# Kernel optimization log

Measured on AMD Instinct MI355X. Metric: run time of the kernel, lower is better.

Reference implementation:

```python
import jax, jax.numpy as jnp
import numpy as np

D_MODEL = 256
N_LEVELS = 4
N_HEADS = 8
N_POINTS = 4
D_HEAD = D_MODEL // N_HEADS  # 32
BATCH = 8
SHAPES = np.array([[64, 64], [32, 32], [16, 16], [8, 8]], dtype=np.int32)
LEN_IN = int((SHAPES[:, 0] * SHAPES[:, 1]).sum())  # 5440
LEN_Q = LEN_IN
STARTS = np.concatenate([[0], np.cumsum(SHAPES[:, 0] * SHAPES[:, 1])[:-1]]).astype(np.int32)


def _offset_bias():
    # faithful _reset_parameters grid init for sampling_offsets bias
    thetas = np.arange(N_HEADS, dtype=np.float64) * (2.0 * np.pi / N_HEADS)
    grid = np.stack([np.cos(thetas), np.sin(thetas)], -1)
    grid = grid / np.abs(grid).max(-1, keepdims=True)
    grid = np.tile(grid[:, None, None, :], (1, N_LEVELS, N_POINTS, 1))
    grid = grid * (np.arange(N_POINTS) + 1)[None, None, :, None]
    return jnp.asarray(grid.reshape(-1), dtype=jnp.float32)


def setup_inputs() -> dict:
    key = jax.random.key(0)
    ks = jax.random.split(key, 8)
    s = 1.0 / np.sqrt(D_MODEL)
    return {
        "query": jax.random.normal(ks[0], (BATCH, LEN_Q, D_MODEL), jnp.float32),
        "reference_points": jax.random.uniform(ks[1], (BATCH, LEN_Q, N_LEVELS, 2), jnp.float32),
        "input_flatten": jax.random.normal(ks[2], (BATCH, LEN_IN, D_MODEL), jnp.float32),
        "input_spatial_shapes": jnp.asarray(SHAPES),
        "input_level_start_index": jnp.asarray(STARTS),
        "W_val": jax.random.normal(ks[3], (D_MODEL, D_MODEL), jnp.float32) * s,
        "b_val": jnp.zeros((D_MODEL,), jnp.float32),
        "W_off": jax.random.normal(ks[4], (D_MODEL, N_HEADS * N_LEVELS * N_POINTS * 2), jnp.float32) * 0.01,
        "b_off": _offset_bias(),
        "W_attn": jax.random.normal(ks[5], (D_MODEL, N_HEADS * N_LEVELS * N_POINTS), jnp.float32) * s,
        "b_attn": jnp.zeros((N_HEADS * N_LEVELS * N_POINTS,), jnp.float32),
        "W_out": jax.random.normal(ks[6], (D_MODEL, D_MODEL), jnp.float32) * s,
        "b_out": jnp.zeros((D_MODEL,), jnp.float32),
    }


def _ms_deform_attn_core(value, shapes_np, starts_np, sampling_locations, attention_weights):
    # value: (N, Lin, Hn, d); sampling_locations: (N, Lq, Hn, L, P, 2) in [0,1]
    # attention_weights: (N, Lq, Hn, L, P)
    n, lq = sampling_locations.shape[:2]
    value_t = jnp.transpose(value, (0, 2, 1, 3))  # (N, Hn, Lin, d)
    out = jnp.zeros((n, N_HEADS, lq, value.shape[-1]), value.dtype)
    for lvl in range(N_LEVELS):
        H, W = int(shapes_np[lvl, 0]), int(shapes_np[lvl, 1])
        st = int(starts_np[lvl])
        v = value_t[:, :, st:st + H * W]  # (N, Hn, H*W, d)
        loc = jnp.transpose(sampling_locations[:, :, :, lvl], (0, 2, 1, 3, 4))  # (N, Hn, Lq, P, 2)
        x = loc[..., 0] * W - 0.5
        y = loc[..., 1] * H - 0.5
        x0 = jnp.floor(x).astype(jnp.int32)
        y0 = jnp.floor(y).astype(jnp.int32)
        lx = x - x0
        ly = y - y0
        x1, y1 = x0 + 1, y0 + 1

        def gather(yc, xc):
            valid = (yc >= 0) & (yc < H) & (xc >= 0) & (xc < W)
            idx = jnp.clip(yc, 0, H - 1) * W + jnp.clip(xc, 0, W - 1)
            idx = idx.reshape(n, N_HEADS, -1)  # (N, Hn, Lq*P)
            g = jnp.take_along_axis(v, idx[..., None], axis=2)  # (N, Hn, Lq*P, d)
            return g * valid.reshape(n, N_HEADS, -1, 1)

        w00 = ((1 - lx) * (1 - ly)).reshape(n, N_HEADS, -1, 1)
        w01 = (lx * (1 - ly)).reshape(n, N_HEADS, -1, 1)
        w10 = ((1 - lx) * ly).reshape(n, N_HEADS, -1, 1)
        w11 = (lx * ly).reshape(n, N_HEADS, -1, 1)
        samp = (gather(y0, x0) * w00 + gather(y0, x1) * w01 +
                gather(y1, x0) * w10 + gather(y1, x1) * w11)
        samp = samp.reshape(n, N_HEADS, lq, N_POINTS, -1)
        aw = jnp.transpose(attention_weights[:, :, :, lvl], (0, 2, 1, 3))  # (N, Hn, Lq, P)
        out = out + (samp * aw[..., None]).sum(axis=3)
    return jnp.transpose(out, (0, 2, 1, 3)).reshape(n, lq, -1)


def reference(query, reference_points, input_flatten, input_spatial_shapes,
              input_level_start_index, W_val, b_val, W_off, b_off,
              W_attn, b_attn, W_out, b_out):
    shapes_np = np.asarray(input_spatial_shapes)
    starts_np = np.asarray(input_level_start_index)
    n, lq, _ = query.shape
    lin = input_flatten.shape[1]

    value = (input_flatten @ W_val + b_val).reshape(n, lin, N_HEADS, D_HEAD)
    off = (query @ W_off + b_off).reshape(n, lq, N_HEADS, N_LEVELS, N_POINTS, 2)
    attn = jax.nn.softmax((query @ W_attn + b_attn).reshape(n, lq, N_HEADS, N_LEVELS * N_POINTS), axis=-1)
    attn = attn.reshape(n, lq, N_HEADS, N_LEVELS, N_POINTS)

    # normalizer: (L, 2) as [W, H]
    normalizer = jnp.stack([input_spatial_shapes[:, 1], input_spatial_shapes[:, 0]], -1).astype(query.dtype)
    loc = reference_points[:, :, None, :, None, :] + off / normalizer[None, None, None, :, None, :]

    out = _ms_deform_attn_core(value, shapes_np, starts_np, loc, attn)
    return out @ W_out + b_out
```

## Files before the change

kernel.cpp:

```cpp
#include <hip/hip_runtime.h>

typedef unsigned short ushort;
typedef unsigned int uint;
typedef __bf16 bf16x8 __attribute__((ext_vector_type(8)));
typedef float floatx4 __attribute__((ext_vector_type(4)));
typedef ushort ushort8 __attribute__((ext_vector_type(8)));

constexpr int LQ = 5440;
constexpr int ROWS = 43520;

__device__ __forceinline__ ushort f2b(float f) {
  union { float f; uint i; } v; v.f = f;
  uint r = v.i + 0x7FFFu + ((v.i >> 16) & 1u);
  return (ushort)(r >> 16);
}
__device__ __forceinline__ float blo(uint u) {
  union { uint i; float f; } v; v.i = u << 16; return v.f;
}
__device__ __forceinline__ float bhi(uint u) {
  union { uint i; float f; } v; v.i = u & 0xFFFF0000u; return v.f;
}

__global__ __launch_bounds__(256) void wcast_kernel(
    const float* __restrict__ Wv, const float* __restrict__ Wo,
    const float* __restrict__ Wa, const float* __restrict__ Wu,
    ushort* __restrict__ Wt) {
  int k = threadIdx.x;
  int n = blockIdx.x;
  int m = blockIdx.y;
  const float* src = (m == 0) ? Wv : (m == 1) ? Wo : (m == 2) ? Wa : Wu;
  int N = (m == 2) ? 128 : 256;
  if (n >= N) return;
  size_t off = (size_t)m * 65536 - ((m == 3) ? 32768 : 0);
  Wt[off + (size_t)n * 256 + k] = f2b(src[(size_t)k * N + n]);
}

template<bool F2B>
__device__ __forceinline__ void tile64_mainloop(
    const void* __restrict__ Av, const ushort* __restrict__ Bt,
    int row_base, int n0, ushort* At, ushort* Bs, floatx4 (&acc)[4][2]) {
  const int t = threadIdx.x;
  const int lane = t & 63, wv = t >> 6;
#pragma unroll
  for (int i = 0; i < 4; ++i)
#pragma unroll
    for (int j = 0; j < 2; ++j) acc[i][j] = floatx4{0.f, 0.f, 0.f, 0.f};

  for (int k0 = 0; k0 < 256; k0 += 32) {
    {
      int r = t >> 2, q = t & 3;
      int slot = ((r >> 4) * 64 + q * 16 + (r & 15)) * 8;
      if (F2B) {
        const float* ap = (const float*)Av + (size_t)(row_base + r) * 256 + k0 + q * 8;
        float4 a0 = *(const float4*)ap, a1 = *(const float4*)(ap + 4);
        ushort8 u;
        u[0] = f2b(a0.x); u[1] = f2b(a0.y); u[2] = f2b(a0.z); u[3] = f2b(a0.w);
        u[4] = f2b(a1.x); u[5] = f2b(a1.y); u[6] = f2b(a1.z); u[7] = f2b(a1.w);
        *(ushort8*)&At[slot] = u;
      } else {
        const ushort* ap = (const ushort*)Av + (size_t)(row_base + r) * 256 + k0 + q * 8;
        *(ushort8*)&At[slot] = *(const ushort8*)ap;
      }
    }
#pragma unroll
    for (int i = 0; i < 2; ++i) {
      int item = t + 256 * i;
      int nr = item >> 2, q = item & 3;
      int slot = ((nr >> 4) * 64 + q * 16 + (nr & 15)) * 8;
      *(ushort8*)&Bs[slot] = *(const ushort8*)(Bt + (size_t)(n0 + nr) * 256 + k0 + q * 8);
    }
    __syncthreads();
    bf16x8 af[4], bf[2];
#pragma unroll
    for (int ti = 0; ti < 4; ++ti)
      af[ti] = *(const bf16x8*)&At[(ti * 64 + lane) * 8];
#pragma unroll
    for (int tjj = 0; tjj < 2; ++tjj)
      bf[tjj] = *(const bf16x8*)&Bs[((2 * wv + tjj) * 64 + lane) * 8];
#pragma unroll
    for (int ti = 0; ti < 4; ++ti)
#pragma unroll
      for (int tjj = 0; tjj < 2; ++tjj)
        acc[ti][tjj] = __builtin_amdgcn_mfma_f32_16x16x32_bf16(af[ti], bf[tjj], acc[ti][tjj], 0, 0, 0);
    __syncthreads();
  }
}

__global__ __launch_bounds__(256) void gemm_val64(
    const float* __restrict__ X, const ushort* __restrict__ WtV,
    const float* __restrict__ bval, ushort* __restrict__ value16) {
  __shared__ ushort At[2048];
  __shared__ ushort Bs[4096];
  floatx4 acc[4][2];
  int row_base = blockIdx.x * 64, n0 = blockIdx.y * 128;
  tile64_mainloop<true>(X, WtV, row_base, n0, At, Bs, acc);
  const int t = threadIdx.x, lane = t & 63, wv = t >> 6;
  const int quad = lane >> 4, l15 = lane & 15;
#pragma unroll
  for (int tjj = 0; tjj < 2; ++tjj) {
    int gcol = n0 + (2 * wv + tjj) * 16 + l15;
    float b = bval[gcol];
#pragma unroll
    for (int ti = 0; ti < 4; ++ti)
#pragma unroll
      for (int reg = 0; reg < 4; ++reg) {
        int grow = row_base + ti * 16 + quad * 4 + reg;
        value16[(size_t)grow * 256 + gcol] = f2b(acc[ti][tjj][reg] + b);
      }
  }
}

__global__ __launch_bounds__(256) void gemm_oa_kernel(
    const float* __restrict__ Q, const ushort* __restrict__ WtOA,
    const float* __restrict__ boff, const float* __restrict__ battn,
    const float* __restrict__ refp, uint4* __restrict__ tblq) {
  __shared__ ushort At[2048];
  __shared__ ushort Bs[3072];
  const int t = threadIdx.x;
  const int lane = t & 63, wv = t >> 6;
  const int quad = lane >> 4, l15 = lane & 15;
  const int bx = blockIdx.x;
  const int row_base = (bx % 680) * 64;
  const int hp = bx / 680;
  floatx4 accO[4], accA[2];
#pragma unroll
  for (int p = 0; p < 4; ++p) accO[p] = floatx4{0.f, 0.f, 0.f, 0.f};
#pragma unroll
  for (int q = 0; q < 2; ++q) accA[q] = floatx4{0.f, 0.f, 0.f, 0.f};

  for (int k0 = 0; k0 < 256; k0 += 32) {
    {
      int r = t >> 2, q = t & 3;
      const float* ap = Q + (size_t)(row_base + r) * 256 + k0 + q * 8;
      float4 a0 = *(const float4*)ap, a1 = *(const float4*)(ap + 4);
      ushort8 u;
      u[0] = f2b(a0.x); u[1] = f2b(a0.y); u[2] = f2b(a0.z); u[3] = f2b(a0.w);
      u[4] = f2b(a1.x); u[5] = f2b(a1.y); u[6] = f2b(a1.z); u[7] = f2b(a1.w);
      *(ushort8*)&At[((r >> 4) * 64 + q * 16 + (r & 15)) * 8] = u;
    }
#pragma unroll
    for (int i = 0; i < 2; ++i) {
      int item = t + 256 * i;
      if (item < 384) {
        int nrl = item >> 2, q = item & 3;
        int grow_ = (nrl < 64) ? (hp * 64 + nrl) : (256 + hp * 32 + (nrl - 64));
        *(ushort8*)&Bs[((nrl >> 4) * 64 + q * 16 + (nrl & 15)) * 8] =
            *(const ushort8*)(WtOA + (size_t)grow_ * 256 + k0 + q * 8);
      }
    }
    __syncthreads();
    bf16x8 af = *(const bf16x8*)&At[(wv * 64 + lane) * 8];
#pragma unroll
    for (int p = 0; p < 4; ++p) {
      bf16x8 bf = *(const bf16x8*)&Bs[(p * 64 + lane) * 8];
      accO[p] = __builtin_amdgcn_mfma_f32_16x16x32_bf16(af, bf, accO[p], 0, 0, 0);
    }
#pragma unroll
    for (int q = 0; q < 2; ++q) {
      bf16x8 bf = *(const bf16x8*)&Bs[((4 + q) * 64 + lane) * 8];
      accA[q] = __builtin_amdgcn_mfma_f32_16x16x32_bf16(af, bf, accA[q], 0, 0, 0);
    }
    __syncthreads();
  }

  const int lp = l15, l = lp >> 2;
  const int wd = 64 >> l;
  const int st = (l == 0) ? 0 : (l == 1) ? 4096 : (l == 2) ? 5120 : 5376;
  const float lw = (float)wd;
  const int src = (quad << 4) | (2 * (lp & 7));
  float boO[4], boA[2];
#pragma unroll
  for (int p = 0; p < 4; ++p) boO[p] = boff[(4 * hp + p) * 16 + l15];
#pragma unroll
  for (int q = 0; q < 2; ++q) boA[q] = battn[(2 * hp + q) * 16 + l15];

#pragma unroll
  for (int reg = 0; reg < 4; ++reg) {
    int grow = row_base + wv * 16 + quad * 4 + reg;
    float rx = refp[(size_t)grow * 8 + l * 2];
    float ry = refp[(size_t)grow * 8 + l * 2 + 1];
#pragma unroll
    for (int hh = 0; hh < 2; ++hh) {
      int h = 2 * hp + hh;
      float xa = accA[hh][reg] + boA[hh];
      float m = xa;
      m = fmaxf(m, __shfl_xor(m, 1, 64));
      m = fmaxf(m, __shfl_xor(m, 2, 64));
      m = fmaxf(m, __shfl_xor(m, 4, 64));
      m = fmaxf(m, __shfl_xor(m, 8, 64));
      float e = __expf(xa - m);
      float ssum = e;
      ssum += __shfl_xor(ssum, 1, 64);
      ssum += __shfl_xor(ssum, 2, 64);
      ssum += __shfl_xor(ssum, 4, 64);
      ssum += __shfl_xor(ssum, 8, 64);
      float aw = e / ssum;
      float v0 = accO[2 * hh][reg] + boO[2 * hh];
      float v1 = accO[2 * hh + 1][reg] + boO[2 * hh + 1];
      float x_lo = __shfl(v0, src, 64),     x_hi = __shfl(v1, src, 64);
      float y_lo = __shfl(v0, src | 1, 64), y_hi = __shfl(v1, src | 1, 64);
      float xo = (lp < 8) ? x_lo : x_hi;
      float yo = (lp < 8) ? y_lo : y_hi;
      float X = rx * lw + xo - 0.5f;
      float Y = ry * lw + yo - 0.5f;
      float fx = floorf(X), fy = floorf(Y);
      float lx = X - fx, ly = Y - fy;
      int x0 = (int)fx, y0 = (int)fy, x1 = x0 + 1, y1 = y0 + 1;
      int cx0 = min(max(x0, 0), wd - 1), cx1 = min(max(x1, 0), wd - 1);
      int cy0 = min(max(y0, 0), wd - 1), cy1 = min(max(y1, 0), wd - 1);
      float vx0 = (x0 >= 0 && x0 < wd) ? 1.f : 0.f;
      float vx1 = (x1 >= 0 && x1 < wd) ? 1.f : 0.f;
      float vy0 = (y0 >= 0 && y0 < wd) ? 1.f : 0.f;
      float vy1 = (y1 >= 0 && y1 < wd) ? 1.f : 0.f;
      float g00 = (1.f - lx) * (1.f - ly) * vx0 * vy0 * aw;
      float g01 = lx * (1.f - ly) * vx1 * vy0 * aw;
      float g10 = (1.f - lx) * ly * vx0 * vy1 * aw;
      float g11 = lx * ly * vx1 * vy1 * aw;
      uint i00 = st + cy0 * wd + cx0, i01 = st + cy0 * wd + cx1;
      uint i10 = st + cy1 * wd + cx0, i11 = st + cy1 * wd + cx1;
      uint4 ov;
      ov.x = i00 | (i01 << 16);
      ov.y = i10 | (i11 << 16);
      ov.z = (uint)f2b(g00) | ((uint)f2b(g01) << 16);
      ov.w = (uint)f2b(g10) | ((uint)f2b(g11) << 16);
      tblq[((size_t)grow * 8 + h) * 16 + lp] = ov;
    }
  }
}

__global__ __launch_bounds__(512) void core_kernel(
    const ushort* __restrict__ value16, const uint4* __restrict__ tblq,
    uint* __restrict__ coreo32) {
  const int bx = blockIdx.x;
  const int b = bx & 7;
  const int pr = bx >> 3;
  const int brow0 = b * LQ + pr * 2;
  const int t = threadIdx.x;
  const int h = t >> 6, lane = t & 63;
  const int s = lane >> 3, g = lane & 7;
  const size_t sb = ((size_t)brow0 * 8 + h) * 16;
  uint4 sA0 = tblq[sb + s];
  uint4 sA1 = tblq[sb + 8 + s];
  uint4 sB0 = tblq[sb + 128 + s];
  uint4 sB1 = tblq[sb + 136 + s];
  const uint2* vb = (const uint2*)value16 + (size_t)b * (LQ * 64) + h * 8 + g;
  float a[4] = {0.f, 0.f, 0.f, 0.f};
  float c[4] = {0.f, 0.f, 0.f, 0.f};

  auto proc = [&](const uint4& sl, float* ac) {
    uint2 v00 = vb[(size_t)(sl.x & 0xFFFFu) * 64];
    uint2 v01 = vb[(size_t)(sl.x >> 16) * 64];
    uint2 v10 = vb[(size_t)(sl.y & 0xFFFFu) * 64];
    uint2 v11 = vb[(size_t)(sl.y >> 16) * 64];
    float w00 = blo(sl.z), w01 = bhi(sl.z), w10 = blo(sl.w), w11 = bhi(sl.w);
    ac[0] = fmaf(w00, blo(v00.x), ac[0]); ac[1] = fmaf(w00, bhi(v00.x), ac[1]);
    ac[2] = fmaf(w00, blo(v00.y), ac[2]); ac[3] = fmaf(w00, bhi(v00.y), ac[3]);
    ac[0] = fmaf(w01, blo(v01.x), ac[0]); ac[1] = fmaf(w01, bhi(v01.x), ac[1]);
    ac[2] = fmaf(w01, blo(v01.y), ac[2]); ac[3] = fmaf(w01, bhi(v01.y), ac[3]);
    ac[0] = fmaf(w10, blo(v10.x), ac[0]); ac[1] = fmaf(w10, bhi(v10.x), ac[1]);
    ac[2] = fmaf(w10, blo(v10.y), ac[2]); ac[3] = fmaf(w10, bhi(v10.y), ac[3]);
    ac[0] = fmaf(w11, blo(v11.x), ac[0]); ac[1] = fmaf(w11, bhi(v11.x), ac[1]);
    ac[2] = fmaf(w11, blo(v11.y), ac[2]); ac[3] = fmaf(w11, bhi(v11.y), ac[3]);
  };
  proc(sA0, a); proc(sA1, a);
  proc(sB0, c); proc(sB1, c);

#pragma unroll
  for (int m = 8; m <= 32; m <<= 1) {
#pragma unroll
    for (int i = 0; i < 4; ++i) {
      a[i] += __shfl_xor(a[i], m, 64);
      c[i] += __shfl_xor(c[i], m, 64);
    }
  }
  if (s == 0) {
    uint2 o0, o1;
    o0.x = (uint)f2b(a[0]) | ((uint)f2b(a[1]) << 16);
    o0.y = (uint)f2b(a[2]) | ((uint)f2b(a[3]) << 16);
    o1.x = (uint)f2b(c[0]) | ((uint)f2b(c[1]) << 16);
    o1.y = (uint)f2b(c[2]) | ((uint)f2b(c[3]) << 16);
    *(uint2*)(coreo32 + (size_t)brow0 * 128 + h * 16 + g * 2) = o0;
    *(uint2*)(coreo32 + (size_t)(brow0 + 1) * 128 + h * 16 + g * 2) = o1;
  }
}

__global__ __launch_bounds__(256) void gemm_out64(
    const ushort* __restrict__ C, const ushort* __restrict__ WtU,
    const float* __restrict__ bout, float* __restrict__ out) {
  __shared__ ushort At[2048];
  __shared__ ushort Bs[4096];
  floatx4 acc[4][2];
  int row_base = blockIdx.x * 64, n0 = blockIdx.y * 128;
  tile64_mainloop<false>(C, WtU, row_base, n0, At, Bs, acc);
  const int t = threadIdx.x, lane = t & 63, wv = t >> 6;
  const int quad = lane >> 4, l15 = lane & 15;
#pragma unroll
  for (int tjj = 0; tjj < 2; ++tjj) {
    int gcol = n0 + (2 * wv + tjj) * 16 + l15;
    float b = bout[gcol];
#pragma unroll
    for (int ti = 0; ti < 4; ++ti)
#pragma unroll
      for (int reg = 0; reg < 4; ++reg) {
        int grow = row_base + ti * 16 + quad * 4 + reg;
        out[(size_t)grow * 256 + gcol] = acc[ti][tjj][reg] + b;
      }
  }
}

extern "C" void kernel_launch(void* const* d_in, const int* in_sizes, int n_in,
                              void* d_out, int out_size, void* d_ws, size_t ws_size,
                              hipStream_t stream) {
  const float* query  = (const float*)d_in[0];
  const float* refp   = (const float*)d_in[1];
  const float* inpf   = (const float*)d_in[2];
  const float* W_val  = (const float*)d_in[5];
  const float* b_val  = (const float*)d_in[6];
  const float* W_off  = (const float*)d_in[7];
  const float* b_off  = (const float*)d_in[8];
  const float* W_attn = (const float*)d_in[9];
  const float* b_attn = (const float*)d_in[10];
  const float* W_out  = (const float*)d_in[11];
  const float* b_out  = (const float*)d_in[12];

  char* ws = (char*)d_ws;
  ushort* Wt    = (ushort*)ws;
  ushort* value = (ushort*)(ws + 1048576);
  uint4*  tbl   = (uint4*)(ws + 23330816);
  ushort* coreo = (ushort*)(ws + 112459776);

  dim3 blk(256);
  wcast_kernel<<<dim3(256, 4), blk, 0, stream>>>(W_val, W_off, W_attn, W_out, Wt);
  gemm_val64  <<<dim3(680, 2), blk, 0, stream>>>(inpf, Wt, b_val, value);
  gemm_oa_kernel<<<dim3(2720), blk, 0, stream>>>(query, Wt + 65536, b_off, b_attn, refp, tbl);
  core_kernel <<<dim3(21760), dim3(512), 0, stream>>>(value, tbl, (uint*)coreo);
  gemm_out64  <<<dim3(680, 2), blk, 0, stream>>>(coreo, Wt + 163840, b_out, (float*)d_out);
}
```

Before: 331.4 us.

## Stage query tile once in LDS and loop head pairs in offset/attn GEMM

The offset/attention GEMM now loads and converts each 64-row query tile to bf16 once into a 32KB LDS buffer. It then loops over the four head pairs inside one block, instead of launching four blocks that each re-read and re-convert the same query rows. Weight tiles are fetched with global_load_lds direct-to-LDS loads, and the A/B staging in the shared 64-tile mainloop uses precomputed pointers with a linear LDS slot layout. The risks are fewer blocks (680 instead of 2720), which lowers parallelism, and larger LDS use per block, which lowers occupancy.

Result: no change. 333.5 us (+0.6%).

```diff
diff --git a/kernel.cpp b/kernel.cpp
--- a/kernel.cpp
+++ b/kernel.cpp
@@ -19,6 +19,11 @@
 }
 __device__ __forceinline__ float bhi(uint u) {
   union { uint i; float f; } v; v.i = u & 0xFFFF0000u; return v.f;
+}
+__device__ __forceinline__ void glds16(const ushort* g, ushort* l) {
+  __builtin_amdgcn_global_load_lds(
+      (const __attribute__((address_space(1))) void*)g,
+      (__attribute__((address_space(3))) void*)l, 16, 0, 0);
 }
 
 __global__ __launch_bounds__(256) void wcast_kernel(
@@ -46,29 +51,31 @@
 #pragma unroll
     for (int j = 0; j < 2; ++j) acc[i][j] = floatx4{0.f, 0.f, 0.f, 0.f};
 
+  const int arow = ((t >> 6) << 4) + (t & 15);
+  const int akoff = ((t >> 4) & 3) * 8;
+  const float* apf = (const float*)Av + (size_t)(row_base + arow) * 256 + akoff;
+  const ushort* aph = (const ushort*)Av + (size_t)(row_base + arow) * 256 + akoff;
+  const ushort* bp[2];
+#pragma unroll
+  for (int i = 0; i < 2; ++i) {
+    int l = t + 256 * i;
+    int nr = ((l >> 6) << 4) + (l & 15);
+    int koff = ((l >> 4) & 3) * 8;
+    bp[i] = Bt + (size_t)(n0 + nr) * 256 + koff;
+  }
+
   for (int k0 = 0; k0 < 256; k0 += 32) {
-    {
-      int r = t >> 2, q = t & 3;
-      int slot = ((r >> 4) * 64 + q * 16 + (r & 15)) * 8;
-      if (F2B) {
-        const float* ap = (const float*)Av + (size_t)(row_base + r) * 256 + k0 + q * 8;
-        float4 a0 = *(const float4*)ap, a1 = *(const float4*)(ap + 4);
-        ushort8 u;
-        u[0] = f2b(a0.x); u[1] = f2b(a0.y); u[2] = f2b(a0.z); u[3] = f2b(a0.w);
-        u[4] = f2b(a1.x); u[5] = f2b(a1.y); u[6] = f2b(a1.z); u[7] = f2b(a1.w);
-        *(ushort8*)&At[slot] = u;
-      } else {
-        const ushort* ap = (const ushort*)Av + (size_t)(row_base + r) * 256 + k0 + q * 8;
-        *(ushort8*)&At[slot] = *(const ushort8*)ap;
-      }
-    }
-#pragma unroll
-    for (int i = 0; i < 2; ++i) {
-      int item = t + 256 * i;
-      int nr = item >> 2, q = item & 3;
-      int slot = ((nr >> 4) * 64 + q * 16 + (nr & 15)) * 8;
-      *(ushort8*)&Bs[slot] = *(const ushort8*)(Bt + (size_t)(n0 + nr) * 256 + k0 + q * 8);
-    }
+    if (F2B) {
+      float4 a0 = *(const float4*)(apf + k0), a1 = *(const float4*)(apf + k0 + 4);
+      ushort8 u;
+      u[0] = f2b(a0.x); u[1] = f2b(a0.y); u[2] = f2b(a0.z); u[3] = f2b(a0.w);
+      u[4] = f2b(a1.x); u[5] = f2b(a1.y); u[6] = f2b(a1.z); u[7] = f2b(a1.w);
+      *(ushort8*)&At[t * 8] = u;
+    } else {
+      *(ushort8*)&At[t * 8] = *(const ushort8*)(aph + k0);
+    }
+    *(ushort8*)&Bs[t * 8] = *(const ushort8*)(bp[0] + k0);
+    *(ushort8*)&Bs[(t + 256) * 8] = *(const ushort8*)(bp[1] + k0);
     __syncthreads();
     bf16x8 af[4], bf[2];
 #pragma unroll
@@ -114,116 +121,144 @@
     const float* __restrict__ Q, const ushort* __restrict__ WtOA,
     const float* __restrict__ boff, const float* __restrict__ battn,
     const float* __restrict__ refp, uint4* __restrict__ tblq) {
-  __shared__ ushort At[2048];
+  __shared__ ushort At[16384];
   __shared__ ushort Bs[3072];
   const int t = threadIdx.x;
   const int lane = t & 63, wv = t >> 6;
   const int quad = lane >> 4, l15 = lane & 15;
-  const int bx = blockIdx.x;
-  const int row_base = (bx % 680) * 64;
-  const int hp = bx / 680;
-  floatx4 accO[4], accA[2];
-#pragma unroll
-  for (int p = 0; p < 4; ++p) accO[p] = floatx4{0.f, 0.f, 0.f, 0.f};
-#pragma unroll
-  for (int q = 0; q < 2; ++q) accA[q] = floatx4{0.f, 0.f, 0.f, 0.f};
-
-  for (int k0 = 0; k0 < 256; k0 += 32) {
-    {
-      int r = t >> 2, q = t & 3;
-      const float* ap = Q + (size_t)(row_base + r) * 256 + k0 + q * 8;
-      float4 a0 = *(const float4*)ap, a1 = *(const float4*)(ap + 4);
+  const int row_base = blockIdx.x * 64;
+
+  {
+    int rowl = ((t >> 6) << 4) + (t & 15);
+    int koff = ((t >> 4) & 3) * 8;
+    const float* ap = Q + (size_t)(row_base + rowl) * 256 + koff;
+#pragma unroll
+    for (int p = 0; p < 8; ++p) {
+      float4 a0 = *(const float4*)(ap + p * 32), a1 = *(const float4*)(ap + p * 32 + 4);
       ushort8 u;
       u[0] = f2b(a0.x); u[1] = f2b(a0.y); u[2] = f2b(a0.z); u[3] = f2b(a0.w);
       u[4] = f2b(a1.x); u[5] = f2b(a1.y); u[6] = f2b(a1.z); u[7] = f2b(a1.w);
-      *(ushort8*)&At[((r >> 4) * 64 + q * 16 + (r & 15)) * 8] = u;
-    }
-#pragma unroll
-    for (int i = 0; i < 2; ++i) {
-      int item = t + 256 * i;
-      if (item < 384) {
-        int nrl = item >> 2, q = item & 3;
-        int grow_ = (nrl < 64) ? (hp * 64 + nrl) : (256 + hp * 32 + (nrl - 64));
-        *(ushort8*)&Bs[((nrl >> 4) * 64 + q * 16 + (nrl & 15)) * 8] =
-            *(const ushort8*)(WtOA + (size_t)grow_ * 256 + k0 + q * 8);
-      }
-    }
-    __syncthreads();
-    bf16x8 af = *(const bf16x8*)&At[(wv * 64 + lane) * 8];
-#pragma unroll
-    for (int p = 0; p < 4; ++p) {
-      bf16x8 bf = *(const bf16x8*)&Bs[(p * 64 + lane) * 8];
-      accO[p] = __builtin_amdgcn_mfma_f32_16x16x32_bf16(af, bf, accO[p], 0, 0, 0);
-    }
-#pragma unroll
-    for (int q = 0; q < 2; ++q) {
-      bf16x8 bf = *(const bf16x8*)&Bs[((4 + q) * 64 + lane) * 8];
-      accA[q] = __builtin_amdgcn_mfma_f32_16x16x32_bf16(af, bf, accA[q], 0, 0, 0);
-    }
-    __syncthreads();
-  }
-
-  const int lp = l15, l = lp >> 2;
-  const int wd = 64 >> l;
-  const int st = (l == 0) ? 0 : (l == 1) ? 4096 : (l == 2) ? 5120 : 5376;
+      *(ushort8*)&At[p * 2048 + t * 8] = u;
+    }
+  }
+
+  const ushort* bsrc0;
+  size_t bstr0;
+  {
+    int nr = ((t >> 6) << 4) + (t & 15);
+    int koff = ((t >> 4) & 3) * 8;
+    bsrc0 = WtOA + (size_t)nr * 256 + koff;
+    bstr0 = (size_t)64 * 256;
+  }
+  const ushort* bsrc1 = nullptr;
+  size_t bstr1 = 0;
+  if (t < 128) {
+    int l = t + 256;
+    int nr = ((l >> 6) << 4) + (l & 15);
+    int koff = ((l >> 4) & 3) * 8;
+    bsrc1 = WtOA + (size_t)(256 + (nr - 64)) * 256 + koff;
+    bstr1 = (size_t)32 * 256;
+  }
+  __syncthreads();
+
+  const int lp = l15, lev = lp >> 2;
+  const int wd = 64 >> lev;
+  const int st = (lev == 0) ? 0 : (lev == 1) ? 4096 : (lev == 2) ? 5120 : 5376;
   const float lw = (float)wd;
   const int src = (quad << 4) | (2 * (lp & 7));
-  float boO[4], boA[2];
-#pragma unroll
-  for (int p = 0; p < 4; ++p) boO[p] = boff[(4 * hp + p) * 16 + l15];
-#pragma unroll
-  for (int q = 0; q < 2; ++q) boA[q] = battn[(2 * hp + q) * 16 + l15];
-
+  float rxs[4], rys[4];
 #pragma unroll
   for (int reg = 0; reg < 4; ++reg) {
     int grow = row_base + wv * 16 + quad * 4 + reg;
-    float rx = refp[(size_t)grow * 8 + l * 2];
-    float ry = refp[(size_t)grow * 8 + l * 2 + 1];
-#pragma unroll
-    for (int hh = 0; hh < 2; ++hh) {
-      int h = 2 * hp + hh;
-      float xa = accA[hh][reg] + boA[hh];
-      float m = xa;
-      m = fmaxf(m, __shfl_xor(m, 1, 64));
-      m = fmaxf(m, __shfl_xor(m, 2, 64));
-      m = fmaxf(m, __shfl_xor(m, 4, 64));
-      m = fmaxf(m, __shfl_xor(m, 8, 64));
-      float e = __expf(xa - m);
-      float ssum = e;
-      ssum += __shfl_xor(ssum, 1, 64);
-      ssum += __shfl_xor(ssum, 2, 64);
-      ssum += __shfl_xor(ssum, 4, 64);
-      ssum += __shfl_xor(ssum, 8, 64);
-      float aw = e / ssum;
-      float v0 = accO[2 * hh][reg] + boO[2 * hh];
-      float v1 = accO[2 * hh + 1][reg] + boO[2 * hh + 1];
-      float x_lo = __shfl(v0, src, 64),     x_hi = __shfl(v1, src, 64);
-      float y_lo = __shfl(v0, src | 1, 64), y_hi = __shfl(v1, src | 1, 64);
-      float xo = (lp < 8) ? x_lo : x_hi;
-      float yo = (lp < 8) ? y_lo : y_hi;
-      float X = rx * lw + xo - 0.5f;
-      float Y = ry * lw + yo - 0.5f;
-      float fx = floorf(X), fy = floorf(Y);
-      float lx = X - fx, ly = Y - fy;
-      int x0 = (int)fx, y0 = (int)fy, x1 = x0 + 1, y1 = y0 + 1;
-      int cx0 = min(max(x0, 0), wd - 1), cx1 = min(max(x1, 0), wd - 1);
-      int cy0 = min(max(y0, 0), wd - 1), cy1 = min(max(y1, 0), wd - 1);
-      float vx0 = (x0 >= 0 && x0 < wd) ? 1.f : 0.f;
-      float vx1 = (x1 >= 0 && x1 < wd) ? 1.f : 0.f;
-      float vy0 = (y0 >= 0 && y0 < wd) ? 1.f : 0.f;
-      float vy1 = (y1 >= 0 && y1 < wd) ? 1.f : 0.f;
-      float g00 = (1.f - lx) * (1.f - ly) * vx0 * vy0 * aw;
-      float g01 = lx * (1.f - ly) * vx1 * vy0 * aw;
-      float g10 = (1.f - lx) * ly * vx0 * vy1 * aw;
-      float g11 = lx * ly * vx1 * vy1 * aw;
-      uint i00 = st + cy0 * wd + cx0, i01 = st + cy0 * wd + cx1;
-      uint i10 = st + cy1 * wd + cx0, i11 = st + cy1 * wd + cx1;
-      uint4 ov;
-      ov.x = i00 | (i01 << 16);
-      ov.y = i10 | (i11 << 16);
-      ov.z = (uint)f2b(g00) | ((uint)f2b(g01) << 16);
-      ov.w = (uint)f2b(g10) | ((uint)f2b(g11) << 16);
-      tblq[((size_t)grow * 8 + h) * 16 + lp] = ov;
+    rxs[reg] = refp[(size_t)grow * 8 + lev * 2];
+    rys[reg] = refp[(size_t)grow * 8 + lev * 2 + 1];
+  }
+
+  for (int hp = 0; hp < 4; ++hp) {
+    floatx4 accO[4], accA[2];
+#pragma unroll
+    for (int p = 0; p < 4; ++p) accO[p] = floatx4{0.f, 0.f, 0.f, 0.f};
+#pragma unroll
+    for (int q = 0; q < 2; ++q) accA[q] = floatx4{0.f, 0.f, 0.f, 0.f};
+
+    const ushort* b0 = bsrc0 + (size_t)hp * bstr0;
+    const ushort* b1 = (t < 128) ? (bsrc1 + (size_t)hp * bstr1) : nullptr;
+
+    for (int p = 0; p < 8; ++p) {
+      glds16(b0 + p * 32, &Bs[t * 8]);
+      if (t < 128) glds16(b1 + p * 32, &Bs[(t + 256) * 8]);
+      __syncthreads();
+      bf16x8 af = *(const bf16x8*)&At[p * 2048 + (wv * 64 + lane) * 8];
+#pragma unroll
+      for (int pp = 0; pp < 4; ++pp) {
+        bf16x8 bf = *(const bf16x8*)&Bs[(pp * 64 + lane) * 8];
+        accO[pp] = __builtin_amdgcn_mfma_f32_16x16x32_bf16(af, bf, accO[pp], 0, 0, 0);
+      }
+#pragma unroll
+      for (int qk = 0; qk < 2; ++qk) {
+        bf16x8 bf = *(const bf16x8*)&Bs[((4 + qk) * 64 + lane) * 8];
+        accA[qk] = __builtin_amdgcn_mfma_f32_16x16x32_bf16(af, bf, accA[qk], 0, 0, 0);
+      }
+      __syncthreads();
+    }
+
+    float boO[4], boA[2];
+#pragma unroll
+    for (int p = 0; p < 4; ++p) boO[p] = boff[(4 * hp + p) * 16 + l15];
+#pragma unroll
+    for (int q = 0; q < 2; ++q) boA[q] = battn[(2 * hp + q) * 16 + l15];
+
+#pragma unroll
+    for (int reg = 0; reg < 4; ++reg) {
+      int grow = row_base + wv * 16 + quad * 4 + reg;
+      float rx = rxs[reg];
+      float ry = rys[reg];
+#pragma unroll
+      for (int hh = 0; hh < 2; ++hh) {
+        int h = 2 * hp + hh;
+        float xa = accA[hh][reg] + boA[hh];
+        float m = xa;
+        m = fmaxf(m, __shfl_xor(m, 1, 64));
+        m = fmaxf(m, __shfl_xor(m, 2, 64));
+        m = fmaxf(m, __shfl_xor(m, 4, 64));
+        m = fmaxf(m, __shfl_xor(m, 8, 64));
+        float e = __expf(xa - m);
+        float ssum = e;
+        ssum += __shfl_xor(ssum, 1, 64);
+        ssum += __shfl_xor(ssum, 2, 64);
+        ssum += __shfl_xor(ssum, 4, 64);
+        ssum += __shfl_xor(ssum, 8, 64);
+        float aw = e / ssum;
+        float v0 = accO[2 * hh][reg] + boO[2 * hh];
+        float v1 = accO[2 * hh + 1][reg] + boO[2 * hh + 1];
+        float x_lo = __shfl(v0, src, 64),     x_hi = __shfl(v1, src, 64);
+        float y_lo = __shfl(v0, src | 1, 64), y_hi = __shfl(v1, src | 1, 64);
+        float xo = (lp < 8) ? x_lo : x_hi;
+        float yo = (lp < 8) ? y_lo : y_hi;
+        float X = rx * lw + xo - 0.5f;
+        float Y = ry * lw + yo - 0.5f;
+        float fx = floorf(X), fy = floorf(Y);
+        float lx = X - fx, ly = Y - fy;
+        int x0 = (int)fx, y0 = (int)fy, x1 = x0 + 1, y1 = y0 + 1;
+        int cx0 = min(max(x0, 0), wd - 1), cx1 = min(max(x1, 0), wd - 1);
+        int cy0 = min(max(y0, 0), wd - 1), cy1 = min(max(y1, 0), wd - 1);
+        float vx0 = (x0 >= 0 && x0 < wd) ? 1.f : 0.f;
+        float vx1 = (x1 >= 0 && x1 < wd) ? 1.f : 0.f;
+        float vy0 = (y0 >= 0 && y0 < wd) ? 1.f : 0.f;
+        float vy1 = (y1 >= 0 && y1 < wd) ? 1.f : 0.f;
+        float g00 = (1.f - lx) * (1.f - ly) * vx0 * vy0 * aw;
+        float g01 = lx * (1.f - ly) * vx1 * vy0 * aw;
+        float g10 = (1.f - lx) * ly * vx0 * vy1 * aw;
+        float g11 = lx * ly * vx1 * vy1 * aw;
+        uint i00 = st + cy0 * wd + cx0, i01 = st + cy0 * wd + cx1;
+        uint i10 = st + cy1 * wd + cx0, i11 = st + cy1 * wd + cx1;
+        uint4 ov;
+        ov.x = i00 | (i01 << 16);
+        ov.y = i10 | (i11 << 16);
+        ov.z = (uint)f2b(g00) | ((uint)f2b(g01) << 16);
+        ov.w = (uint)f2b(g10) | ((uint)f2b(g11) << 16);
+        tblq[((size_t)grow * 8 + h) * 16 + lp] = ov;
+      }
     }
   }
 }
@@ -332,7 +367,7 @@
   dim3 blk(256);
   wcast_kernel<<<dim3(256, 4), blk, 0, stream>>>(W_val, W_off, W_attn, W_out, Wt);
   gemm_val64  <<<dim3(680, 2), blk, 0, stream>>>(inpf, Wt, b_val, value);
-  gemm_oa_kernel<<<dim3(2720), blk, 0, stream>>>(query, Wt + 65536, b_off, b_attn, refp, tbl);
+  gemm_oa_kernel<<<dim3(680), blk, 0, stream>>>(query, Wt + 65536, b_off, b_attn, refp, tbl);
   core_kernel <<<dim3(21760), dim3(512), 0, stream>>>(value, tbl, (uint*)coreo);
   gemm_out64  <<<dim3(680, 2), blk, 0, stream>>>(coreo, Wt + 163840, b_out, (float*)d_out);
 }
```
